# Performance work log

Measured on AMD Instinct MI355X. Metric: run time of the kernel, lower is better.

Reference implementation:

```python
import jax, jax.numpy as jnp
import numpy as np

B, H, S, D = 4, 16, 2048, 64

def setup_inputs() -> dict:
    key = jax.random.key(0)
    kq, kk, kv = jax.random.split(key, 3)
    Q = jax.random.normal(kq, (B, H, S, D), dtype=jnp.float32)
    K = jax.random.normal(kk, (B, H, S, D), dtype=jnp.float32)
    V = jax.random.normal(kv, (B, H, S, D), dtype=jnp.float32)
    return {"Q": Q, "K": K, "V": V}

def reference(Q, K, V):
    d_model = Q.shape[-1]
    # [B,H,S,S] scores matrix, materialized as in the original (unfused SDPA)
    scores = jnp.einsum('bhqd,bhkd->bhqk', Q, K) / jnp.sqrt(jnp.float32(d_model))
    attention = jax.nn.softmax(scores, axis=-1)
    out = jnp.einsum('bhqk,bhkd->bhqd', attention, V)
    return out
```

## Files before the change

### kernel.cpp

```cpp
#include <hip/hip_runtime.h>
#include <hip/hip_bf16.h>

namespace {

constexpr int kSeq = 2048;
constexpr int kD   = 64;
constexpr int kBH  = 64;
constexpr int kQB  = 256;
constexpr int kBN  = 64;
constexpr int kNT  = kSeq / kBN;
constexpr int kGrid = kBH * (kSeq / kQB);
constexpr int kPs  = 72;

typedef __attribute__((ext_vector_type(8))) short bf16x8;
typedef __attribute__((ext_vector_type(4))) float f32x4;
typedef __attribute__((ext_vector_type(2))) unsigned int u32x2;

__device__ __forceinline__ unsigned short f2bf(float f) {
  unsigned int u = __builtin_bit_cast(unsigned int, f);
  u += 0x7fffu + ((u >> 16) & 1u);
  return (unsigned short)(u >> 16);
}

__device__ __forceinline__ unsigned int pkbf(float a, float b) {
#if __has_builtin(__builtin_amdgcn_cvt_pk_bf16_f32)
  typedef __attribute__((ext_vector_type(2))) __bf16 bfv2;
  bfv2 r = __builtin_amdgcn_cvt_pk_bf16_f32(a, b);
  return __builtin_bit_cast(unsigned int, r);
#else
  unsigned int ua = __builtin_bit_cast(unsigned int, a) + 0x8000u;
  unsigned int ub = __builtin_bit_cast(unsigned int, b) + 0x8000u;
  return __builtin_amdgcn_perm(ub, ua, 0x07060302);
#endif
}

__device__ __forceinline__ float fexp2(float x) {
#if __has_builtin(__builtin_amdgcn_exp2f)
  return __builtin_amdgcn_exp2f(x);
#else
  return exp2f(x);
#endif
}

__device__ __forceinline__ void load16(const unsigned short* g, unsigned short* l) {
  __builtin_amdgcn_global_load_lds(
      (const __attribute__((address_space(1))) unsigned int*)g,
      (__attribute__((address_space(3))) unsigned int*)l, 16, 0, 0);
}

__global__ __launch_bounds__(256) void prep(
    const float* __restrict__ K, const float* __restrict__ V,
    unsigned short* __restrict__ Kbf, unsigned short* __restrict__ Vt) {
  __shared__ float sTf[kD * 65];
  const int tid = threadIdx.x;
  const int bh = blockIdx.x >> 5;
  const int t0 = (blockIdx.x & 31) * 64;
  const float* Kb = K + ((size_t)bh * kSeq + t0) * kD;
  const float* Vb = V + ((size_t)bh * kSeq + t0) * kD;
  unsigned short* Ko = Kbf + ((size_t)bh * kSeq + t0) * kD;
#pragma unroll
  for (int t = 0; t < 4; ++t) {
    const int idx = tid + t * 256;
    const int row = idx >> 4;
    const int c4  = (idx & 15) * 4;
    const float4 k4 = *(const float4*)(Kb + row * kD + c4);
    u32x2 kp = {pkbf(k4.x, k4.y), pkbf(k4.z, k4.w)};
    *(u32x2*)(Ko + row * kD + c4) = kp;
    const float4 v4 = *(const float4*)(Vb + row * kD + c4);
    sTf[(c4 + 0) * 65 + row] = v4.x;
    sTf[(c4 + 1) * 65 + row] = v4.y;
    sTf[(c4 + 2) * 65 + row] = v4.z;
    sTf[(c4 + 3) * 65 + row] = v4.w;
  }
  __syncthreads();
  const int d = tid >> 2, q = tid & 3;
  const float* ts = &sTf[d * 65 + q * 16];
  float p[16];
#pragma unroll
  for (int j = 0; j < 16; ++j) p[j] = ts[j];
  uint4 a, b;
  a.x = pkbf(p[0], p[1]);   a.y = pkbf(p[2], p[3]);
  a.z = pkbf(p[4], p[5]);   a.w = pkbf(p[6], p[7]);
  b.x = pkbf(p[8], p[9]);   b.y = pkbf(p[10], p[11]);
  b.z = pkbf(p[12], p[13]); b.w = pkbf(p[14], p[15]);
  unsigned short* vo = Vt + ((size_t)bh * kD + d) * kSeq + t0 + q * 16;
  *(uint4*)(vo)     = a;
  *(uint4*)(vo + 8) = b;
}

__global__ __launch_bounds__(512, 4) void fattn8(
    const float* __restrict__ Q, const unsigned short* __restrict__ Kbf,
    const unsigned short* __restrict__ Vt, float* __restrict__ O) {
  __shared__ unsigned short sK[2][kBN * kD];
  __shared__ unsigned short sV[2][kD * kBN];
  __shared__ unsigned short sP[8 * 32 * kD];

  const int tid  = threadIdx.x;
  const int wave = tid >> 6;
  const int lane = tid & 63;
  const int quad = lane >> 4;
  const int l16  = lane & 15;
  const int swz  = l16 & 7;

  const int x  = blockIdx.x & 7;
  const int j  = blockIdx.x >> 3;
  const int bh = x * 8 + (j >> 3);
  const int q0 = (j & 7) * kQB;
  const size_t kb = (size_t)bh * kSeq * kD;

  constexpr float cs = 0.18033688011112042f;

  bf16x8 qf[2][2];
#pragma unroll
  for (int mt = 0; mt < 2; ++mt) {
    const float* qr =
        Q + kb + (size_t)(q0 + wave * 32 + mt * 16 + l16) * kD + quad * 8;
#pragma unroll
    for (int kc = 0; kc < 2; ++kc)
#pragma unroll
      for (int jj = 0; jj < 8; ++jj)
        qf[mt][kc][jj] = (short)f2bf(qr[kc * 32 + jj] * cs);
  }

  bf16x8 ones;
#pragma unroll
  for (int jj = 0; jj < 8; ++jj) ones[jj] = (short)0x3F80;

  const int r0 = tid >> 3, c0 = (tid & 7) ^ (r0 & 7);
  const unsigned short* kg0 = Kbf + kb + r0 * kD + c0 * 8;
  const unsigned short* vg0 = Vt + kb + r0 * kSeq + c0 * 8;

  f32x4 o[2][4];
#pragma unroll
  for (int mt = 0; mt < 2; ++mt)
#pragma unroll
    for (int dt = 0; dt < 4; ++dt) o[mt][dt] = (f32x4){0.f, 0.f, 0.f, 0.f};
  f32x4 lacc[2] = {(f32x4){0.f, 0.f, 0.f, 0.f}, (f32x4){0.f, 0.f, 0.f, 0.f}};

  unsigned short* pwA = &sP[(wave * 32 + l16) * kD];
  unsigned short* pwB = pwA + 16 * kD;

  load16(kg0, &sK[0][tid * 8]);
  load16(vg0, &sV[0][tid * 8]);

  for (int t = 0; t < kNT; ++t) {
    const int p = t & 1;
    __syncthreads();
    if (t + 1 < kNT) {
      const int pn = p ^ 1;
      const size_t ko = (size_t)(t + 1) * kBN * kD;
      const int vo = (t + 1) * kBN;
      load16(kg0 + ko, &sK[pn][tid * 8]);
      load16(vg0 + vo, &sV[pn][tid * 8]);
    }
    const unsigned short* sKp = sK[p];
    const unsigned short* sVp = sV[p];

    f32x4 sA[4], sB[4];
#pragma unroll
    for (int nt = 0; nt < 4; ++nt) {
      sA[nt] = (f32x4){0.f, 0.f, 0.f, 0.f};
      sB[nt] = (f32x4){0.f, 0.f, 0.f, 0.f};
    }
    __builtin_amdgcn_s_setprio(1);
#pragma unroll
    for (int kc = 0; kc < 2; ++kc)
#pragma unroll
      for (int nt = 0; nt < 4; ++nt) {
        const bf16x8 kf = *(const bf16x8*)&sKp[(nt * 16 + l16) * kD +
                                              (((kc * 4 + quad) ^ swz) * 8)];
        sA[nt] = __builtin_amdgcn_mfma_f32_16x16x32_bf16(kf, qf[0][kc], sA[nt], 0, 0, 0);
        sB[nt] = __builtin_amdgcn_mfma_f32_16x16x32_bf16(kf, qf[1][kc], sB[nt], 0, 0, 0);
      }
    __builtin_amdgcn_s_setprio(0);

#pragma unroll
    for (int nt = 0; nt < 4; ++nt) {
      const int pc = ((nt * 2 + (quad >> 1)) ^ swz) * 8 + (quad & 1) * 4;
      u32x2 ppA = {pkbf(fexp2(sA[nt][0]), fexp2(sA[nt][1])),
                   pkbf(fexp2(sA[nt][2]), fexp2(sA[nt][3]))};
      *(u32x2*)&pwA[pc] = ppA;
      u32x2 ppB = {pkbf(fexp2(sB[nt][0]), fexp2(sB[nt][1])),
                   pkbf(fexp2(sB[nt][2]), fexp2(sB[nt][3]))};
      *(u32x2*)&pwB[pc] = ppB;
    }

    __builtin_amdgcn_s_setprio(1);
#pragma unroll
    for (int kc = 0; kc < 2; ++kc) {
      const int ac = ((kc * 4 + quad) ^ swz) * 8;
      const bf16x8 afA = *(const bf16x8*)&pwA[ac];
      const bf16x8 afB = *(const bf16x8*)&pwB[ac];
      lacc[0] = __builtin_amdgcn_mfma_f32_16x16x32_bf16(afA, ones, lacc[0], 0, 0, 0);
      lacc[1] = __builtin_amdgcn_mfma_f32_16x16x32_bf16(afB, ones, lacc[1], 0, 0, 0);
#pragma unroll
      for (int dt = 0; dt < 4; ++dt) {
        const bf16x8 vf = *(const bf16x8*)&sVp[(dt * 16 + l16) * kBN + ac];
        o[0][dt] = __builtin_amdgcn_mfma_f32_16x16x32_bf16(afA, vf, o[0][dt], 0, 0, 0);
        o[1][dt] = __builtin_amdgcn_mfma_f32_16x16x32_bf16(afB, vf, o[1][dt], 0, 0, 0);
      }
    }
    __builtin_amdgcn_s_setprio(0);
  }

#pragma unroll
  for (int mt = 0; mt < 2; ++mt) {
    float* Ob = O + kb + (size_t)(q0 + wave * 32 + mt * 16) * kD;
#pragma unroll
    for (int r = 0; r < 4; ++r) {
      const float inv = 1.f / lacc[mt][r];
#pragma unroll
      for (int dt = 0; dt < 4; ++dt)
        Ob[(quad * 4 + r) * kD + dt * 16 + l16] = o[mt][dt][r] * inv;
    }
  }
}

__global__ __launch_bounds__(256, 4) void fattn_fb(
    const float* __restrict__ Q, const float* __restrict__ K,
    const float* __restrict__ V, float* __restrict__ O) {
  __shared__ unsigned short sK[kBN * kPs];
  __shared__ unsigned short sV[kD * kPs];
  __shared__ unsigned short sP[4 * 16 * kPs];
  const int tid = threadIdx.x, wave = tid >> 6, lane = tid & 63;
  const int quad = lane >> 4, l16 = lane & 15;
  const int bh = blockIdx.x >> 5, q0 = (blockIdx.x & 31) * 64;
  const float* Qb = Q + (size_t)bh * kSeq * kD;
  const float* Kb = K + (size_t)bh * kSeq * kD;
  const float* Vb = V + (size_t)bh * kSeq * kD;
  bf16x8 qf[2];
  {
    const float* qr = Qb + (size_t)(q0 + wave * 16 + l16) * kD + quad * 8;
#pragma unroll
    for (int kc = 0; kc < 2; ++kc)
#pragma unroll
      for (int jj = 0; jj < 8; ++jj) qf[kc][jj] = (short)f2bf(qr[kc * 32 + jj]);
  }
  f32x4 o[4];
#pragma unroll
  for (int dt = 0; dt < 4; ++dt) o[dt] = (f32x4){0.f, 0.f, 0.f, 0.f};
  float lsum[4] = {0.f, 0.f, 0.f, 0.f};
  constexpr float cs = 0.18033688011112042f;
  unsigned short* pw = &sP[wave * 16 * kPs];
  for (int kv0 = 0; kv0 < kSeq; kv0 += kBN) {
    __syncthreads();
#pragma unroll
    for (int t = 0; t < 4; ++t) {
      const int idx = tid + t * 256;
      const int row = idx >> 4, c4 = (idx & 15) * 4;
      const float4 k4 = *(const float4*)(Kb + (size_t)(kv0 + row) * kD + c4);
      unsigned short* kd = &sK[row * kPs + c4];
      kd[0] = f2bf(k4.x); kd[1] = f2bf(k4.y); kd[2] = f2bf(k4.z); kd[3] = f2bf(k4.w);
      const float4 v4 = *(const float4*)(Vb + (size_t)(kv0 + row) * kD + c4);
      sV[(c4 + 0) * kPs + row] = f2bf(v4.x);
      sV[(c4 + 1) * kPs + row] = f2bf(v4.y);
      sV[(c4 + 2) * kPs + row] = f2bf(v4.z);
      sV[(c4 + 3) * kPs + row] = f2bf(v4.w);
    }
    __syncthreads();
    f32x4 s[4];
#pragma unroll
    for (int nt = 0; nt < 4; ++nt) s[nt] = (f32x4){0.f, 0.f, 0.f, 0.f};
#pragma unroll
    for (int kc = 0; kc < 2; ++kc)
#pragma unroll
      for (int nt = 0; nt < 4; ++nt) {
        const bf16x8 kf = *(const bf16x8*)&sK[(nt * 16 + l16) * kPs + kc * 32 + quad * 8];
        s[nt] = __builtin_amdgcn_mfma_f32_16x16x32_bf16(qf[kc], kf, s[nt], 0, 0, 0);
      }
#pragma unroll
    for (int nt = 0; nt < 4; ++nt)
#pragma unroll
      for (int r = 0; r < 4; ++r) {
        const float p = fexp2(s[nt][r] * cs);
        lsum[r] += p;
        pw[(quad * 4 + r) * kPs + nt * 16 + l16] = f2bf(p);
      }
#pragma unroll
    for (int kc = 0; kc < 2; ++kc) {
      const bf16x8 af = *(const bf16x8*)&pw[l16 * kPs + kc * 32 + quad * 8];
#pragma unroll
      for (int dt = 0; dt < 4; ++dt) {
        const bf16x8 vf = *(const bf16x8*)&sV[(dt * 16 + l16) * kPs + kc * 32 + quad * 8];
        o[dt] = __builtin_amdgcn_mfma_f32_16x16x32_bf16(af, vf, o[dt], 0, 0, 0);
      }
    }
  }
#pragma unroll
  for (int r = 0; r < 4; ++r)
#pragma unroll
    for (int off = 1; off < 16; off <<= 1)
      lsum[r] += __shfl_xor(lsum[r], off, 64);
  float* Ob = O + (size_t)bh * kSeq * kD + (size_t)(q0 + wave * 16) * kD;
#pragma unroll
  for (int r = 0; r < 4; ++r) {
    const float inv = 1.f / lsum[r];
#pragma unroll
    for (int dt = 0; dt < 4; ++dt)
      Ob[(quad * 4 + r) * kD + dt * 16 + l16] = o[dt][r] * inv;
  }
}

}

extern "C" void kernel_launch(void* const* d_in, const int* in_sizes, int n_in,
                              void* d_out, int out_size, void* d_ws, size_t ws_size,
                              hipStream_t stream) {
  const float* Q = (const float*)d_in[0];
  const float* K = (const float*)d_in[1];
  const float* V = (const float*)d_in[2];
  float* Oo = (float*)d_out;
  const size_t need = (size_t)2 * kBH * kSeq * kD * sizeof(unsigned short);
  if (ws_size >= need) {
    unsigned short* Kbf = (unsigned short*)d_ws;
    unsigned short* Vt  = Kbf + (size_t)kBH * kSeq * kD;
    prep<<<dim3(kBH * (kSeq / 64)), dim3(256), 0, stream>>>(K, V, Kbf, Vt);
    fattn8<<<dim3(kGrid), dim3(512), 0, stream>>>(Q, Kbf, Vt, Oo);
  } else {
    fattn_fb<<<dim3(kBH * (kSeq / 64)), dim3(256), 0, stream>>>(Q, K, V, Oo);
  }
}
```

Before: 201.7 us.

## Use 4 waves with 64 query rows each instead of 8 waves with 32

Restructures the attention kernel from 8 waves of 32 query rows to 4 waves of 64 query rows per 256-row block. Each K/V fragment read from LDS now feeds four MFMA row tiles instead of two, which cuts LDS read traffic per FLOP, and each thread loads two chunks per tile. The cost is more accumulator registers per wave (16 score tiles plus 16 output tiles), lower occupancy (launch bounds 256,2) and fewer waves available to hide latency.

Result: slower. 207.7 us (+3.0%).

```diff
diff --git a/kernel.cpp b/kernel.cpp
--- a/kernel.cpp
+++ b/kernel.cpp
@@ -88,12 +88,12 @@
   *(uint4*)(vo + 8) = b;
 }
 
-__global__ __launch_bounds__(512, 4) void fattn8(
+__global__ __launch_bounds__(256, 2) void fattn4(
     const float* __restrict__ Q, const unsigned short* __restrict__ Kbf,
     const unsigned short* __restrict__ Vt, float* __restrict__ O) {
   __shared__ unsigned short sK[2][kBN * kD];
   __shared__ unsigned short sV[2][kD * kBN];
-  __shared__ unsigned short sP[8 * 32 * kD];
+  __shared__ unsigned short sP[4 * 64 * kD];
 
   const int tid  = threadIdx.x;
   const int wave = tid >> 6;
@@ -110,11 +110,11 @@
 
   constexpr float cs = 0.18033688011112042f;
 
-  bf16x8 qf[2][2];
-#pragma unroll
-  for (int mt = 0; mt < 2; ++mt) {
+  bf16x8 qf[4][2];
+#pragma unroll
+  for (int mt = 0; mt < 4; ++mt) {
     const float* qr =
-        Q + kb + (size_t)(q0 + wave * 32 + mt * 16 + l16) * kD + quad * 8;
+        Q + kb + (size_t)(q0 + wave * 64 + mt * 16 + l16) * kD + quad * 8;
 #pragma unroll
     for (int kc = 0; kc < 2; ++kc)
 #pragma unroll
@@ -126,22 +126,29 @@
 #pragma unroll
   for (int jj = 0; jj < 8; ++jj) ones[jj] = (short)0x3F80;
 
-  const int r0 = tid >> 3, c0 = (tid & 7) ^ (r0 & 7);
+  const int i0 = tid, i1 = tid + 256;
+  const int r0 = i0 >> 3, c0 = (i0 & 7) ^ (r0 & 7);
+  const int r1 = i1 >> 3, c1 = (i1 & 7) ^ (r1 & 7);
   const unsigned short* kg0 = Kbf + kb + r0 * kD + c0 * 8;
+  const unsigned short* kg1 = Kbf + kb + r1 * kD + c1 * 8;
   const unsigned short* vg0 = Vt + kb + r0 * kSeq + c0 * 8;
-
-  f32x4 o[2][4];
-#pragma unroll
-  for (int mt = 0; mt < 2; ++mt)
+  const unsigned short* vg1 = Vt + kb + r1 * kSeq + c1 * 8;
+
+  f32x4 o[4][4];
+#pragma unroll
+  for (int mt = 0; mt < 4; ++mt)
 #pragma unroll
     for (int dt = 0; dt < 4; ++dt) o[mt][dt] = (f32x4){0.f, 0.f, 0.f, 0.f};
-  f32x4 lacc[2] = {(f32x4){0.f, 0.f, 0.f, 0.f}, (f32x4){0.f, 0.f, 0.f, 0.f}};
-
-  unsigned short* pwA = &sP[(wave * 32 + l16) * kD];
-  unsigned short* pwB = pwA + 16 * kD;
-
-  load16(kg0, &sK[0][tid * 8]);
-  load16(vg0, &sV[0][tid * 8]);
+  f32x4 lacc[4];
+#pragma unroll
+  for (int mt = 0; mt < 4; ++mt) lacc[mt] = (f32x4){0.f, 0.f, 0.f, 0.f};
+
+  unsigned short* pw0 = &sP[(wave * 64 + l16) * kD];
+
+  load16(kg0, &sK[0][i0 * 8]);
+  load16(kg1, &sK[0][i1 * 8]);
+  load16(vg0, &sV[0][i0 * 8]);
+  load16(vg1, &sV[0][i1 * 8]);
 
   for (int t = 0; t < kNT; ++t) {
     const int p = t & 1;
@@ -150,18 +157,19 @@
       const int pn = p ^ 1;
       const size_t ko = (size_t)(t + 1) * kBN * kD;
       const int vo = (t + 1) * kBN;
-      load16(kg0 + ko, &sK[pn][tid * 8]);
-      load16(vg0 + vo, &sV[pn][tid * 8]);
+      load16(kg0 + ko, &sK[pn][i0 * 8]);
+      load16(kg1 + ko, &sK[pn][i1 * 8]);
+      load16(vg0 + vo, &sV[pn][i0 * 8]);
+      load16(vg1 + vo, &sV[pn][i1 * 8]);
     }
     const unsigned short* sKp = sK[p];
     const unsigned short* sVp = sV[p];
 
-    f32x4 sA[4], sB[4];
-#pragma unroll
-    for (int nt = 0; nt < 4; ++nt) {
-      sA[nt] = (f32x4){0.f, 0.f, 0.f, 0.f};
-      sB[nt] = (f32x4){0.f, 0.f, 0.f, 0.f};
-    }
+    f32x4 s[4][4];
+#pragma unroll
+    for (int mt = 0; mt < 4; ++mt)
+#pragma unroll
+      for (int nt = 0; nt < 4; ++nt) s[mt][nt] = (f32x4){0.f, 0.f, 0.f, 0.f};
     __builtin_amdgcn_s_setprio(1);
 #pragma unroll
     for (int kc = 0; kc < 2; ++kc)
@@ -169,43 +177,51 @@
       for (int nt = 0; nt < 4; ++nt) {
         const bf16x8 kf = *(const bf16x8*)&sKp[(nt * 16 + l16) * kD +
                                               (((kc * 4 + quad) ^ swz) * 8)];
-        sA[nt] = __builtin_amdgcn_mfma_f32_16x16x32_bf16(kf, qf[0][kc], sA[nt], 0, 0, 0);
-        sB[nt] = __builtin_amdgcn_mfma_f32_16x16x32_bf16(kf, qf[1][kc], sB[nt], 0, 0, 0);
+#pragma unroll
+        for (int mt = 0; mt < 4; ++mt)
+          s[mt][nt] =
+              __builtin_amdgcn_mfma_f32_16x16x32_bf16(kf, qf[mt][kc], s[mt][nt], 0, 0, 0);
       }
     __builtin_amdgcn_s_setprio(0);
 
 #pragma unroll
-    for (int nt = 0; nt < 4; ++nt) {
-      const int pc = ((nt * 2 + (quad >> 1)) ^ swz) * 8 + (quad & 1) * 4;
-      u32x2 ppA = {pkbf(fexp2(sA[nt][0]), fexp2(sA[nt][1])),
-                   pkbf(fexp2(sA[nt][2]), fexp2(sA[nt][3]))};
-      *(u32x2*)&pwA[pc] = ppA;
-      u32x2 ppB = {pkbf(fexp2(sB[nt][0]), fexp2(sB[nt][1])),
-                   pkbf(fexp2(sB[nt][2]), fexp2(sB[nt][3]))};
-      *(u32x2*)&pwB[pc] = ppB;
+    for (int mt = 0; mt < 4; ++mt) {
+      unsigned short* pw = pw0 + mt * 16 * kD;
+#pragma unroll
+      for (int nt = 0; nt < 4; ++nt) {
+        const int pc = ((nt * 2 + (quad >> 1)) ^ swz) * 8 + (quad & 1) * 4;
+        u32x2 pp = {pkbf(fexp2(s[mt][nt][0]), fexp2(s[mt][nt][1])),
+                    pkbf(fexp2(s[mt][nt][2]), fexp2(s[mt][nt][3]))};
+        *(u32x2*)&pw[pc] = pp;
+      }
     }
 
     __builtin_amdgcn_s_setprio(1);
 #pragma unroll
     for (int kc = 0; kc < 2; ++kc) {
       const int ac = ((kc * 4 + quad) ^ swz) * 8;
-      const bf16x8 afA = *(const bf16x8*)&pwA[ac];
-      const bf16x8 afB = *(const bf16x8*)&pwB[ac];
-      lacc[0] = __builtin_amdgcn_mfma_f32_16x16x32_bf16(afA, ones, lacc[0], 0, 0, 0);
-      lacc[1] = __builtin_amdgcn_mfma_f32_16x16x32_bf16(afB, ones, lacc[1], 0, 0, 0);
+      bf16x8 af[4];
+#pragma unroll
+      for (int mt = 0; mt < 4; ++mt)
+        af[mt] = *(const bf16x8*)&pw0[mt * 16 * kD + ac];
+#pragma unroll
+      for (int mt = 0; mt < 4; ++mt)
+        lacc[mt] = __builtin_amdgcn_mfma_f32_16x16x32_bf16(af[mt], ones, lacc[mt], 0, 0, 0);
 #pragma unroll
       for (int dt = 0; dt < 4; ++dt) {
         const bf16x8 vf = *(const bf16x8*)&sVp[(dt * 16 + l16) * kBN + ac];
-        o[0][dt] = __builtin_amdgcn_mfma_f32_16x16x32_bf16(afA, vf, o[0][dt], 0, 0, 0);
-        o[1][dt] = __builtin_amdgcn_mfma_f32_16x16x32_bf16(afB, vf, o[1][dt], 0, 0, 0);
+#pragma unroll
+        for (int mt = 0; mt < 4; ++mt)
+          o[mt][dt] =
+              __builtin_amdgcn_mfma_f32_16x16x32_bf16(af[mt], vf, o[mt][dt], 0, 0, 0);
       }
     }
     __builtin_amdgcn_s_setprio(0);
   }
 
 #pragma unroll
-  for (int mt = 0; mt < 2; ++mt) {
-    float* Ob = O + kb + (size_t)(q0 + wave * 32 + mt * 16) * kD;
+  for (int mt = 0; mt < 4; ++mt) {
+    float* Ob = O + kb + (size_t)(q0 + wave * 64 + mt * 16) * kD;
 #pragma unroll
     for (int r = 0; r < 4; ++r) {
       const float inv = 1.f / lacc[mt][r];
@@ -315,7 +331,7 @@
     unsigned short* Kbf = (unsigned short*)d_ws;
     unsigned short* Vt  = Kbf + (size_t)kBH * kSeq * kD;
     prep<<<dim3(kBH * (kSeq / 64)), dim3(256), 0, stream>>>(K, V, Kbf, Vt);
-    fattn8<<<dim3(kGrid), dim3(512), 0, stream>>>(Q, Kbf, Vt, Oo);
+    fattn4<<<dim3(kGrid), dim3(256), 0, stream>>>(Q, Kbf, Vt, Oo);
   } else {
     fattn_fb<<<dim3(kBH * (kSeq / 64)), dim3(256), 0, stream>>>(Q, K, V, Oo);
   }
```
